# Optimization experiments

Measured on AMD Instinct MI355X. Metric: run time of the kernel, lower is better.

The kernel has to match this reference:

```python
import jax, jax.numpy as jnp
import numpy as np

NUM_EMBEDDINGS = 512
EMBEDDING_DIM = 64
COMMITMENT_COST = 0.25


def setup_inputs() -> dict:
    key = jax.random.key(0)
    k1, k2 = jax.random.split(key)
    inputs = jax.random.normal(k1, (32, EMBEDDING_DIM, 64, 64), dtype=jnp.float32)
    # nn.Embedding weight init: uniform(-1/K, 1/K)
    weight = jax.random.uniform(
        k2, (NUM_EMBEDDINGS, EMBEDDING_DIM), dtype=jnp.float32,
        minval=-1.0 / NUM_EMBEDDINGS, maxval=1.0 / NUM_EMBEDDINGS)
    return {"inputs": inputs, "weight": weight}


def reference(inputs, weight):
    # NCHW -> NHWC
    x = jnp.transpose(inputs, (0, 2, 3, 1))
    B, H, W, D = x.shape
    flat = x.reshape(-1, D)  # [N, D]
    # squared L2 distances to each code: [N, K]
    distances = (jnp.sum(flat * flat, axis=1, keepdims=True)
                 - 2.0 * flat @ weight.T
                 + jnp.sum(weight * weight, axis=1))
    idx = jnp.argmin(distances, axis=1)  # [N]
    # one-hot @ weight == gather (one-hot entries are exactly 0/1)
    quantized = jnp.take(weight, idx, axis=0).reshape(B, H, W, D)
    e_latent_loss = jnp.mean((jax.lax.stop_gradient(quantized) - x) ** 2)
    q_latent_loss = jnp.mean((quantized - jax.lax.stop_gradient(x)) ** 2)
    loss = q_latent_loss + COMMITMENT_COST * e_latent_loss
    # straight-through estimator
    quantized_st = x + jax.lax.stop_gradient(quantized - x)
    discrete_latent = idx.reshape(B, H, W)
    quantized_out = jnp.transpose(quantized_st, (0, 3, 1, 2))  # NHWC -> NCHW
    return discrete_latent, quantized_out, loss
```

## Files before the change

### kernel.cpp

```cpp
#include <hip/hip_runtime.h>

typedef unsigned long long ull;

#define NUM_K   512
#define DIM     64
#define N_ROWS  (32 * 64 * 64)
#define HW      4096
#define CHW     (64 * 4096)

#define IDX_OFF  0
#define Q_OFF    N_ROWS
#define LOSS_OFF (N_ROWS + 32 * 64 * 4096)

#define TILE_R  256
#define RS      68
#define CAP     8

#define WK1S    1.0e-4f
#define WK2S    2.0e-5f

#define WS_FRAG_LO   16384
#define WS_W2_OFF    32768
#define WS_SW_OFF    33280
#define WS_LSL_BYTE  135168
#define WS_NEED      139264

typedef __attribute__((ext_vector_type(8))) short bf16x8;
typedef __attribute__((ext_vector_type(4))) float f32x4;

#define NP_SUMSQ64(SRC, DST)                                                   \
    do {                                                                       \
        float r_[8];                                                           \
        _Pragma("unroll")                                                      \
        for (int j_ = 0; j_ < 8; ++j_) r_[j_] = __fmul_rn((SRC)[j_], (SRC)[j_]); \
        _Pragma("unroll")                                                      \
        for (int i_ = 8; i_ < 64; i_ += 8) {                                   \
            _Pragma("unroll")                                                  \
            for (int j_ = 0; j_ < 8; ++j_)                                     \
                r_[j_] = __fadd_rn(r_[j_], __fmul_rn((SRC)[i_ + j_], (SRC)[i_ + j_])); \
        }                                                                      \
        (DST) = __fadd_rn(__fadd_rn(__fadd_rn(r_[0], r_[1]), __fadd_rn(r_[2], r_[3])), \
                          __fadd_rn(__fadd_rn(r_[4], r_[5]), __fadd_rn(r_[6], r_[7]))); \
    } while (0)

__device__ __forceinline__ unsigned bf16rn(float f) {
    unsigned u = __float_as_uint(f);
    return (u + 0x7fffu + ((u >> 16) & 1u)) >> 16;
}
__device__ __forceinline__ float bf2f(unsigned h) { return __uint_as_float(h << 16); }
__device__ __forceinline__ unsigned pk2(float lo, float hi) {
    return bf16rn(lo) | (bf16rn(hi) << 16);
}

__device__ __forceinline__ float evald(const float* __restrict__ xr,
                                       const float* __restrict__ wc,
                                       float A, float w2c) {
    float m = 0.0f;
    #pragma unroll
    for (int d = 0; d < DIM; ++d) m = __fmaf_rn(xr[d], wc[d], m);
    return __fadd_rn(__fsub_rn(A, __fmul_rn(2.0f, m)), w2c);
}

__global__ void vq_prep(const float* __restrict__ weight, unsigned* __restrict__ ws) {
    const int c = blockIdx.x * 64 + threadIdx.x;
    const float* wr = weight + c * DIM;
    float wv[DIM];
    #pragma unroll
    for (int d = 0; d < DIM; d += 4) {
        float4 t4 = *(const float4*)&wr[d];
        wv[d] = t4.x; wv[d + 1] = t4.y; wv[d + 2] = t4.z; wv[d + 3] = t4.w;
    }
    float s; NP_SUMSQ64(wv, s);
    ((float*)(ws + WS_W2_OFF))[c] = s;
    float sa = 0.0f;
    #pragma unroll
    for (int d = 0; d < DIM; ++d) sa = __fadd_rn(sa, fabsf(wv[d]));
    ((float*)(ws + WS_SW_OFF))[c] = sa * 1.0002f + 1e-7f;

    const int tb = (c >> 4) * 512;
    const int ls = (c & 15) * 4;
    #pragma unroll
    for (int g = 0; g < 8; ++g) {
        int base = tb + (g >> 2) * 256 + (g & 3) * 64 + ls;
        unsigned hu[4], lu[4];
        #pragma unroll
        for (int p = 0; p < 4; ++p) {
            float e0 = wv[8 * g + 2 * p], e1 = wv[8 * g + 2 * p + 1];
            unsigned h0 = bf16rn(e0), h1 = bf16rn(e1);
            float r0 = __fsub_rn(e0, bf2f(h0));
            float r1 = __fsub_rn(e1, bf2f(h1));
            hu[p] = h0 | (h1 << 16);
            lu[p] = bf16rn(r0) | (bf16rn(r1) << 16);
        }
        *(uint4*)&ws[base] = make_uint4(hu[0], hu[1], hu[2], hu[3]);
        *(uint4*)&ws[WS_FRAG_LO + base] = make_uint4(lu[0], lu[1], lu[2], lu[3]);
    }
}

__global__ __launch_bounds__(512, 4) void vq_mfma2(const float* __restrict__ x_in,
                                                   const float* __restrict__ weight,
                                                   const unsigned* __restrict__ frg,
                                                   const float* __restrict__ w2g,
                                                   const float* __restrict__ swg,
                                                   double* __restrict__ lslots,
                                                   float* __restrict__ out) {
    __shared__ float xlds[TILE_R * RS];
    __shared__ float Arow[TILE_R];
    __shared__ float maxx[TILE_R];
    __shared__ int   cntL[TILE_R];
    __shared__ unsigned short listL[TILE_R * CAP];
    __shared__ int   ilds[TILE_R];
    __shared__ float wsum[8];

    const int tid   = threadIdx.x;
    const int lane  = tid & 63;
    const int wid   = tid >> 6;
    const int wbase = wid * 32;
    const int qid   = lane >> 4;
    const int l15   = lane & 15;

    const int rowbase = blockIdx.x * TILE_R;
    const int b       = rowbase >> 12;
    const int hw0     = rowbase & 4095;
    const float* xb   = x_in + (size_t)b * CHW + hw0;

    #pragma unroll
    for (int it = 0; it < 8; ++it) {
        int e = it * 512 + tid;
        int d = e >> 6, r4 = (e & 63) << 2;
        float4 v = *(const float4*)(xb + d * HW + r4);
        xlds[(r4 + 0) * RS + d] = v.x;
        xlds[(r4 + 1) * RS + d] = v.y;
        xlds[(r4 + 2) * RS + d] = v.z;
        xlds[(r4 + 3) * RS + d] = v.w;
    }
    if (tid < TILE_R) cntL[tid] = 0;
    __syncthreads();

    if (tid < TILE_R) {
        const float* src = &xlds[tid * RS];
        float s; NP_SUMSQ64(src, s);
        Arow[tid] = s;
        float mx = 0.0f;
        #pragma unroll
        for (int d = 0; d < DIM; ++d) mx = fmaxf(mx, fabsf(src[d]));
        maxx[tid] = mx;
    }

    bf16x8 afh[2][2], afl[2][2];
    #pragma unroll
    for (int rt = 0; rt < 2; ++rt) {
        int r = wbase + 16 * rt + l15;
        #pragma unroll
        for (int h = 0; h < 2; ++h) {
            int kb = h * 32 + qid * 8;
            float4 xa = *(const float4*)&xlds[r * RS + kb];
            float4 xc = *(const float4*)&xlds[r * RS + kb + 4];
            float xs[8] = {xa.x, xa.y, xa.z, xa.w, xc.x, xc.y, xc.z, xc.w};
            union { unsigned u[4]; bf16x8 v; } ch, cl;
            #pragma unroll
            for (int p = 0; p < 4; ++p) {
                float e0 = xs[2 * p], e1 = xs[2 * p + 1];
                unsigned h0 = bf16rn(e0), h1 = bf16rn(e1);
                float r0 = __fsub_rn(e0, bf2f(h0));
                float r1 = __fsub_rn(e1, bf2f(h1));
                ch.u[p] = h0 | (h1 << 16);
                cl.u[p] = bf16rn(r0) | (bf16rn(r1) << 16);
            }
            afh[rt][h] = ch.v;
            afl[rt][h] = cl.v;
        }
    }
    __syncthreads();

    float wk1r[2][4], tmin[2][4];
    #pragma unroll
    for (int rt = 0; rt < 2; ++rt)
        #pragma unroll
        for (int rg = 0; rg < 4; ++rg) {
            wk1r[rt][rg] = WK1S * maxx[wbase + 16 * rt + 4 * qid + rg];
            tmin[rt][rg] = 3.4e38f;
        }

    const unsigned* fh  = frg + lane * 4;
    const unsigned* flo = frg + WS_FRAG_LO + lane * 4;
    float swrun = 0.0f;

    for (int q = 0; q < 4; ++q) {
        #pragma unroll
        for (int sc = 0; sc < 2; ++sc) {
            f32x4 acc[2][4] = {};
            #pragma unroll
            for (int jx = 0; jx < 4; ++jx) {
                const int tb2 = ((q * 2 + sc) * 4 + jx) * 512;
                bf16x8 bh0 = *(const bf16x8*)&fh[tb2];
                bf16x8 bh1 = *(const bf16x8*)&fh[tb2 + 256];
                bf16x8 bl0 = *(const bf16x8*)&flo[tb2];
                bf16x8 bl1 = *(const bf16x8*)&flo[tb2 + 256];
                #pragma unroll
                for (int rt = 0; rt < 2; ++rt) {
                    acc[rt][jx] = __builtin_amdgcn_mfma_f32_16x16x32_bf16(afh[rt][0], bh0, acc[rt][jx], 0, 0, 0);
                    acc[rt][jx] = __builtin_amdgcn_mfma_f32_16x16x32_bf16(afh[rt][1], bh1, acc[rt][jx], 0, 0, 0);
                    acc[rt][jx] = __builtin_amdgcn_mfma_f32_16x16x32_bf16(afl[rt][0], bh0, acc[rt][jx], 0, 0, 0);
                    acc[rt][jx] = __builtin_amdgcn_mfma_f32_16x16x32_bf16(afl[rt][1], bh1, acc[rt][jx], 0, 0, 0);
                    acc[rt][jx] = __builtin_amdgcn_mfma_f32_16x16x32_bf16(afh[rt][0], bl0, acc[rt][jx], 0, 0, 0);
                    acc[rt][jx] = __builtin_amdgcn_mfma_f32_16x16x32_bf16(afh[rt][1], bl1, acc[rt][jx], 0, 0, 0);
                }
            }

            float tl[2][4], swv[4], swm = 0.0f;
            #pragma unroll
            for (int rt = 0; rt < 2; ++rt)
                #pragma unroll
                for (int rg = 0; rg < 4; ++rg) tl[rt][rg] = 3.4e38f;
            #pragma unroll
            for (int jx = 0; jx < 4; ++jx) {
                int c = q * 128 + (sc * 4 + jx) * 16 + l15;
                float w2hv = 0.5f * w2g[c];
                float sv = swg[c];
                swv[jx] = sv; swm = fmaxf(swm, sv);
                #pragma unroll
                for (int rt = 0; rt < 2; ++rt)
                    #pragma unroll
                    for (int rg = 0; rg < 4; ++rg) {
                        float t = __fsub_rn(w2hv, acc[rt][jx][rg]);
                        acc[rt][jx][rg] = t;
                        tl[rt][rg] = fminf(tl[rt][rg], t);
                    }
            }
            #pragma unroll
            for (int mk = 1; mk <= 8; mk <<= 1) {
                #pragma unroll
                for (int rt = 0; rt < 2; ++rt)
                    #pragma unroll
                    for (int rg = 0; rg < 4; ++rg)
                        tl[rt][rg] = fminf(tl[rt][rg], __shfl_xor(tl[rt][rg], mk));
                swm = fmaxf(swm, __shfl_xor(swm, mk));
            }
            swrun = fmaxf(swrun, swm);
            #pragma unroll
            for (int rt = 0; rt < 2; ++rt)
                #pragma unroll
                for (int rg = 0; rg < 4; ++rg)
                    tmin[rt][rg] = fminf(tmin[rt][rg], tl[rt][rg]);

            #pragma unroll
            for (int rt = 0; rt < 2; ++rt)
                #pragma unroll
                for (int rg = 0; rg < 4; ++rg) {
                    float gate = __fmaf_rn(wk1r[rt][rg], swm + swrun, tmin[rt][rg] + WK2S);
                    if (tl[rt][rg] <= gate) {
                        #pragma unroll
                        for (int jx = 0; jx < 4; ++jx) {
                            float thr = __fmaf_rn(wk1r[rt][rg], swv[jx] + swrun, tmin[rt][rg] + WK2S);
                            if (acc[rt][jx][rg] <= thr) {
                                int r = wbase + 16 * rt + 4 * qid + rg;
                                int c = q * 128 + (sc * 4 + jx) * 16 + l15;
                                int cn = atomicAdd(&cntL[r], 1);
                                if (cn < CAP) listL[r * CAP + cn] = (unsigned short)c;
                            }
                        }
                    }
                }
        }
    }

    __syncthreads();

    if (lane < 32) {
        const int r   = wbase + lane;
        const int cnt = cntL[r];
        if (cnt >= 1 && cnt <= CAP) {
            int bi;
            if (cnt == 1) {
                bi = listL[r * CAP];
            } else {
                const float* xr = &xlds[r * RS];
                const float  A  = Arow[r];
                float bd = 3.4e38f; bi = 1 << 30;
                for (int t2 = 0; t2 < cnt; ++t2) {
                    int c = listL[r * CAP + t2];
                    float d2 = evald(xr, weight + c * DIM, A, w2g[c]);
                    if (d2 < bd || (d2 == bd && c < bi)) { bd = d2; bi = c; }
                }
            }
            ilds[r] = bi;
            out[IDX_OFF + rowbase + r] = (float)bi;
        }
    }
    for (int rr = 0; rr < 32; ++rr) {
        int r   = wbase + rr;
        int cnt = cntL[r];
        if (cnt < 1 || cnt > CAP) {
            const float* xr = &xlds[r * RS];
            const float  A  = Arow[r];
            float bd = 3.4e38f; int bi = 1 << 30;
            #pragma unroll
            for (int t2 = 0; t2 < 8; ++t2) {
                int c = t2 * 64 + lane;
                float d2 = evald(xr, weight + c * DIM, A, w2g[c]);
                if (d2 < bd || (d2 == bd && c < bi)) { bd = d2; bi = c; }
            }
            ull key = ((ull)__float_as_uint(bd) << 32) | (unsigned)bi;
            #pragma unroll
            for (int mk = 1; mk <= 32; mk <<= 1) {
                ull o = __shfl_xor(key, mk);
                if (o < key) key = o;
            }
            if (lane == 0) {
                int bi2 = (int)(key & 0xffffffffu);
                ilds[r] = bi2;
                out[IDX_OFF + rowbase + r] = (float)bi2;
            }
        }
    }
    __syncthreads();

    const int row = wbase + (lane & 31);
    const int dh  = (lane >> 5) << 5;
    const float* xr2 = &xlds[row * RS + dh];
    const float* wr2 = weight + ilds[row] * DIM + dh;
    float* ob = out + Q_OFF + (size_t)b * CHW + hw0 + row;
    float lsum = 0.0f;
    #pragma unroll
    for (int t2 = 0; t2 < 8; ++t2) {
        float4 xv  = *(const float4*)&xr2[4 * t2];
        float4 wv2 = *(const float4*)&wr2[4 * t2];
        float dd;
        dd = __fsub_rn(wv2.x, xv.x); ob[(size_t)(dh + 4 * t2 + 0) * HW] = __fadd_rn(xv.x, dd); lsum = fmaf(dd, dd, lsum);
        dd = __fsub_rn(wv2.y, xv.y); ob[(size_t)(dh + 4 * t2 + 1) * HW] = __fadd_rn(xv.y, dd); lsum = fmaf(dd, dd, lsum);
        dd = __fsub_rn(wv2.z, xv.z); ob[(size_t)(dh + 4 * t2 + 2) * HW] = __fadd_rn(xv.z, dd); lsum = fmaf(dd, dd, lsum);
        dd = __fsub_rn(wv2.w, xv.w); ob[(size_t)(dh + 4 * t2 + 3) * HW] = __fadd_rn(xv.w, dd); lsum = fmaf(dd, dd, lsum);
    }
    #pragma unroll
    for (int off = 32; off > 0; off >>= 1) lsum += __shfl_down(lsum, off);
    if (lane == 0) wsum[wid] = lsum;
    __syncthreads();
    if (tid == 0) {
        double s = 0.0;
        #pragma unroll
        for (int i = 0; i < 8; ++i) s += (double)wsum[i];
        lslots[blockIdx.x] = s;
    }
}

__global__ void vq_finalize4(const double* __restrict__ lslots,
                             float* __restrict__ out) {
    double s = 0.0;
    for (int i = threadIdx.x; i < 512; i += 64) s += lslots[i];
    #pragma unroll
    for (int off = 32; off > 0; off >>= 1) s += __shfl_down(s, off);
    if (threadIdx.x == 0) {
        double m = s / 8388608.0;
        out[LOSS_OFF] = (float)(m + 0.25 * m);
    }
}

#define R1RS      68
#define R1CAP     16
#define WK1       0.018f
#define WK2       2.5e-4f

__global__ __launch_bounds__(512, 2) void vq_mfma(const float* __restrict__ x_in,
                                                  const float* __restrict__ weight,
                                                  double* __restrict__ lslots,
                                                  float* __restrict__ out) {
    __shared__ float xlds[TILE_R * R1RS];
    __shared__ unsigned bfr[NUM_K * 32];
    __shared__ float w2all[NUM_K];
    __shared__ float w2h[NUM_K];
    __shared__ float sumw[NUM_K];
    __shared__ float Arow[TILE_R];
    __shared__ float maxx[TILE_R];
    __shared__ int   cntL[TILE_R];
    __shared__ unsigned short listL[TILE_R * R1CAP];
    __shared__ int   ilds[TILE_R];
    __shared__ float wsum[8];

    const int tid   = threadIdx.x;
    const int lane  = tid & 63;
    const int wid   = tid >> 6;
    const int wbase = wid * 32;
    const int qid   = lane >> 4;
    const int l15   = lane & 15;

    const int rowbase = blockIdx.x * TILE_R;
    const int b       = rowbase >> 12;
    const int hw0     = rowbase & 4095;
    const float* xb   = x_in + (size_t)b * CHW + hw0;

    #pragma unroll
    for (int it = 0; it < 8; ++it) {
        int id  = it * 512 + tid;
        int row = id & 255, g = id >> 8;
        const float* gp = xb + g * 4 * HW + row;
        float4 v = make_float4(gp[0], gp[HW], gp[2 * HW], gp[3 * HW]);
        *(float4*)&xlds[row * R1RS + g * 4] = v;
    }
    {
        const int c = tid;
        const float* wr = weight + c * DIM;
        float wv[DIM];
        #pragma unroll
        for (int d = 0; d < DIM; d += 4) {
            float4 t4 = *(const float4*)&wr[d];
            wv[d] = t4.x; wv[d + 1] = t4.y; wv[d + 2] = t4.z; wv[d + 3] = t4.w;
        }
        float s; NP_SUMSQ64(wv, s);
        w2all[c] = s;
        w2h[c]   = 0.5f * s;
        float sa = 0.0f;
        #pragma unroll
        for (int d = 0; d < DIM; ++d) sa = __fadd_rn(sa, fabsf(wv[d]));
        sumw[c] = sa * 1.0002f + 1e-7f;
        const int tb = (c >> 4) * 512;
        const int ls = (c & 15) * 4;
        #pragma unroll
        for (int g = 0; g < 8; ++g) {
            int base = tb + (g >> 2) * 256 + (g & 3) * 64 + ls;
            uint4 pw = make_uint4(pk2(wv[8 * g + 0], wv[8 * g + 1]),
                                  pk2(wv[8 * g + 2], wv[8 * g + 3]),
                                  pk2(wv[8 * g + 4], wv[8 * g + 5]),
                                  pk2(wv[8 * g + 6], wv[8 * g + 7]));
            *(uint4*)&bfr[base] = pw;
        }
    }
    if (tid < TILE_R) cntL[tid] = 0;
    __syncthreads();

    if (tid < TILE_R) {
        const float* src = &xlds[tid * R1RS];
        float s; NP_SUMSQ64(src, s);
        Arow[tid] = s;
        float mx = 0.0f;
        #pragma unroll
        for (int d = 0; d < DIM; ++d) mx = fmaxf(mx, fabsf(src[d]));
        maxx[tid] = mx;
    }

    bf16x8 afr[2][2];
    #pragma unroll
    for (int rt = 0; rt < 2; ++rt) {
        int r = wbase + 16 * rt + l15;
        #pragma unroll
        for (int h = 0; h < 2; ++h) {
            int kb = h * 32 + qid * 8;
            float4 xa  = *(const float4*)&xlds[r * R1RS + kb];
            float4 xc  = *(const float4*)&xlds[r * R1RS + kb + 4];
            union { unsigned u[4]; bf16x8 v; } cv;
            cv.u[0] = pk2(xa.x, xa.y); cv.u[1] = pk2(xa.z, xa.w);
            cv.u[2] = pk2(xc.x, xc.y); cv.u[3] = pk2(xc.z, xc.w);
            afr[rt][h] = cv.v;
        }
    }
    __syncthreads();

    float wk1r[2][4], tmin[2][4];
    #pragma unroll
    for (int rt = 0; rt < 2; ++rt)
        #pragma unroll
        for (int rg = 0; rg < 4; ++rg) {
            wk1r[rt][rg] = WK1 * maxx[wbase + 16 * rt + 4 * qid + rg];
            tmin[rt][rg] = 3.4e38f;
        }

    const int lane4 = lane * 4;
    for (int q = 0; q < 4; ++q) {
        f32x4 acc[2][8] = {};
        #pragma unroll
        for (int j = 0; j < 8; ++j) {
            int tb2 = (q * 8 + j) * 512;
            bf16x8 bb0 = *(const bf16x8*)&bfr[tb2 + lane4];
            bf16x8 bb1 = *(const bf16x8*)&bfr[tb2 + 256 + lane4];
            acc[0][j] = __builtin_amdgcn_mfma_f32_16x16x32_bf16(afr[0][0], bb0, acc[0][j], 0, 0, 0);
            acc[0][j] = __builtin_amdgcn_mfma_f32_16x16x32_bf16(afr[0][1], bb1, acc[0][j], 0, 0, 0);
            acc[1][j] = __builtin_amdgcn_mfma_f32_16x16x32_bf16(afr[1][0], bb0, acc[1][j], 0, 0, 0);
            acc[1][j] = __builtin_amdgcn_mfma_f32_16x16x32_bf16(afr[1][1], bb1, acc[1][j], 0, 0, 0);
        }

        const int k0 = q * 128;
        float swv[8], tl[2][4];
        #pragma unroll
        for (int rt = 0; rt < 2; ++rt)
            #pragma unroll
            for (int rg = 0; rg < 4; ++rg) tl[rt][rg] = 3.4e38f;
        #pragma unroll
        for (int j = 0; j < 8; ++j) {
            int c = k0 + j * 16 + l15;
            float w2hv = w2h[c];
            swv[j] = sumw[c];
            #pragma unroll
            for (int rt = 0; rt < 2; ++rt)
                #pragma unroll
                for (int rg = 0; rg < 4; ++rg) {
                    float t = w2hv - acc[rt][j][rg];
                    acc[rt][j][rg] = t;
                    tl[rt][rg] = fminf(tl[rt][rg], t);
                }
        }
        #pragma unroll
        for (int mk = 1; mk <= 8; mk <<= 1)
            #pragma unroll
            for (int rt = 0; rt < 2; ++rt)
                #pragma unroll
                for (int rg = 0; rg < 4; ++rg)
                    tl[rt][rg] = fminf(tl[rt][rg], __shfl_xor(tl[rt][rg], mk));
        float thr0[2][4];
        #pragma unroll
        for (int rt = 0; rt < 2; ++rt)
            #pragma unroll
            for (int rg = 0; rg < 4; ++rg) {
                tmin[rt][rg] = fminf(tmin[rt][rg], tl[rt][rg]);
                thr0[rt][rg] = tmin[rt][rg] + WK2;
            }
        float swmax = swv[0];
        #pragma unroll
        for (int j = 1; j < 8; ++j) swmax = fmaxf(swmax, swv[j]);

        #pragma unroll
        for (int rt = 0; rt < 2; ++rt)
            #pragma unroll
            for (int rg = 0; rg < 4; ++rg) {
                if (tl[rt][rg] <= __fmaf_rn(wk1r[rt][rg], swmax, thr0[rt][rg])) {
                    #pragma unroll
                    for (int j = 0; j < 8; ++j) {
                        if (acc[rt][j][rg] <= __fmaf_rn(wk1r[rt][rg], swv[j], thr0[rt][rg])) {
                            int r  = wbase + 16 * rt + 4 * qid + rg;
                            int c  = k0 + j * 16 + l15;
                            int cn = atomicAdd(&cntL[r], 1);
                            if (cn < R1CAP) listL[r * R1CAP + cn] = (unsigned short)c;
                        }
                    }
                }
            }
    }

    __syncthreads();

    if (lane < 32) {
        const int r   = wbase + lane;
        const int cnt = cntL[r];
        if (cnt >= 1 && cnt <= R1CAP) {
            const float* xr = &xlds[r * R1RS];
            const float  A  = Arow[r];
            float bd = 3.4e38f; int bi = 1 << 30;
            for (int t2 = 0; t2 < cnt; ++t2) {
                int c = listL[r * R1CAP + t2];
                float d2 = evald(xr, weight + c * DIM, A, w2all[c]);
                if (d2 < bd || (d2 == bd && c < bi)) { bd = d2; bi = c; }
            }
            ilds[r] = bi;
            out[IDX_OFF + rowbase + r] = (float)bi;
        }
    }
    for (int rr = 0; rr < 32; ++rr) {
        int r   = wbase + rr;
        int cnt = cntL[r];
        if (cnt < 1 || cnt > R1CAP) {
            const float* xr = &xlds[r * R1RS];
            const float  A  = Arow[r];
            float bd = 3.4e38f; int bi = 1 << 30;
            #pragma unroll
            for (int t2 = 0; t2 < 8; ++t2) {
                int c = t2 * 64 + lane;
                float d2 = evald(xr, weight + c * DIM, A, w2all[c]);
                if (d2 < bd || (d2 == bd && c < bi)) { bd = d2; bi = c; }
            }
            ull key = ((ull)__float_as_uint(bd) << 32) | (unsigned)bi;
            #pragma unroll
            for (int mk = 1; mk <= 32; mk <<= 1) {
                ull o = __shfl_xor(key, mk);
                if (o < key) key = o;
            }
            if (lane == 0) {
                int bi2 = (int)(key & 0xffffffffu);
                ilds[r] = bi2;
                out[IDX_OFF + rowbase + r] = (float)bi2;
            }
        }
    }
    __syncthreads();

    const int row = wbase + (lane & 31);
    const int dh  = (lane >> 5) << 5;
    const float* xr2 = &xlds[row * R1RS + dh];
    const float* wr2 = weight + ilds[row] * DIM + dh;
    float* ob = out + Q_OFF + (size_t)b * CHW + hw0 + row;
    float lsum = 0.0f;
    #pragma unroll
    for (int t2 = 0; t2 < 8; ++t2) {
        float4 xv  = *(const float4*)&xr2[4 * t2];
        float4 wv2 = *(const float4*)&wr2[4 * t2];
        float dd;
        dd = __fsub_rn(wv2.x, xv.x); ob[(size_t)(dh + 4 * t2 + 0) * HW] = __fadd_rn(xv.x, dd); lsum = fmaf(dd, dd, lsum);
        dd = __fsub_rn(wv2.y, xv.y); ob[(size_t)(dh + 4 * t2 + 1) * HW] = __fadd_rn(xv.y, dd); lsum = fmaf(dd, dd, lsum);
        dd = __fsub_rn(wv2.z, xv.z); ob[(size_t)(dh + 4 * t2 + 2) * HW] = __fadd_rn(xv.z, dd); lsum = fmaf(dd, dd, lsum);
        dd = __fsub_rn(wv2.w, xv.w); ob[(size_t)(dh + 4 * t2 + 3) * HW] = __fadd_rn(xv.w, dd); lsum = fmaf(dd, dd, lsum);
    }
    #pragma unroll
    for (int off = 32; off > 0; off >>= 1) lsum += __shfl_down(lsum, off);
    if (lane == 0) wsum[wid] = lsum;
    __syncthreads();
    if (tid == 0) {
        double s = 0.0;
        #pragma unroll
        for (int i = 0; i < 8; ++i) s += (double)wsum[i];
        lslots[blockIdx.x] = s;
    }
}

__global__ void vq_zero(double* __restrict__ loss_acc) {
    if (threadIdx.x == 0) *loss_acc = 0.0;
}

__global__ __launch_bounds__(256) void vq_fused(const float* __restrict__ x_in,
                                                const float* __restrict__ weight,
                                                double* __restrict__ loss_acc,
                                                float* __restrict__ out) {
    __shared__ float w2s[NUM_K];
    for (int k = threadIdx.x; k < NUM_K; k += 256) {
        const float* wk = weight + k * DIM;
        float s; NP_SUMSQ64(wk, s);
        w2s[k] = s;
    }
    __syncthreads();

    const int n  = blockIdx.x * 256 + threadIdx.x;
    const int b  = n >> 12;
    const int hw = n & 4095;
    const float* xp = x_in + b * CHW + hw;
    float x[DIM];
    #pragma unroll
    for (int d = 0; d < DIM; ++d) x[d] = xp[d * HW];

    float A; NP_SUMSQ64(x, A);

    float best = 3.4e38f;
    int   bi   = 0;
    for (int k = 0; k < NUM_K; k += 4) {
        const float* w0 = weight + k * DIM;
        float m0 = 0.f, m1 = 0.f, m2 = 0.f, m3 = 0.f;
        #pragma unroll
        for (int d = 0; d < DIM; ++d) {
            float xd = x[d];
            m0 = __fmaf_rn(xd, w0[d],           m0);
            m1 = __fmaf_rn(xd, w0[DIM + d],     m1);
            m2 = __fmaf_rn(xd, w0[2 * DIM + d], m2);
            m3 = __fmaf_rn(xd, w0[3 * DIM + d], m3);
        }
        float d0 = __fadd_rn(__fsub_rn(A, __fmul_rn(2.0f, m0)), w2s[k]);
        float d1 = __fadd_rn(__fsub_rn(A, __fmul_rn(2.0f, m1)), w2s[k + 1]);
        float d2 = __fadd_rn(__fsub_rn(A, __fmul_rn(2.0f, m2)), w2s[k + 2]);
        float d3 = __fadd_rn(__fsub_rn(A, __fmul_rn(2.0f, m3)), w2s[k + 3]);
        if (d0 < best) { best = d0; bi = k; }
        if (d1 < best) { best = d1; bi = k + 1; }
        if (d2 < best) { best = d2; bi = k + 2; }
        if (d3 < best) { best = d3; bi = k + 3; }
    }
    const int idx = bi;

    out[IDX_OFF + n] = (float)idx;
    const float* qrow = weight + idx * DIM;
    float* oq = out + Q_OFF + b * CHW + hw;
    float lsum = 0.0f;
    #pragma unroll
    for (int d = 0; d < DIM; ++d) {
        float xd   = xp[d * HW];
        float diff = __fsub_rn(qrow[d], xd);
        oq[d * HW] = __fadd_rn(xd, diff);
        lsum = fmaf(diff, diff, lsum);
    }
    #pragma unroll
    for (int off = 32; off > 0; off >>= 1) lsum += __shfl_down(lsum, off);
    __shared__ float wsum[4];
    if ((threadIdx.x & 63) == 0) wsum[threadIdx.x >> 6] = lsum;
    __syncthreads();
    if (threadIdx.x == 0)
        atomicAdd(loss_acc, (double)((wsum[0] + wsum[1]) + (wsum[2] + wsum[3])));
}

__global__ void vq_finalize(const double* __restrict__ loss_acc,
                            float* __restrict__ out) {
    double m = *loss_acc / 8388608.0;
    out[LOSS_OFF] = (float)(m + 0.25 * m);
}

extern "C" void kernel_launch(void* const* d_in, const int* in_sizes, int n_in,
                              void* d_out, int out_size, void* d_ws, size_t ws_size,
                              hipStream_t stream) {
    const float* x = (const float*)d_in[0];
    const float* w = (const float*)d_in[1];
    float* out = (float*)d_out;

    if (ws_size >= WS_NEED) {
        unsigned* ws32 = (unsigned*)d_ws;
        const float* w2g = (const float*)(ws32 + WS_W2_OFF);
        const float* swg = (const float*)(ws32 + WS_SW_OFF);
        double* lslots = (double*)((char*)d_ws + WS_LSL_BYTE);
        vq_prep<<<8, 64, 0, stream>>>(w, ws32);
        vq_mfma2<<<N_ROWS / TILE_R, 512, 0, stream>>>(x, w, ws32, w2g, swg, lslots, out);
        vq_finalize4<<<1, 64, 0, stream>>>(lslots, out);
    } else if (ws_size >= 512 * sizeof(double)) {
        double* lslots = (double*)d_ws;
        vq_mfma<<<N_ROWS / TILE_R, 512, 0, stream>>>(x, w, lslots, out);
        vq_finalize4<<<1, 64, 0, stream>>>(lslots, out);
    } else {
        double* loss_acc = (double*)d_ws;
        vq_zero<<<1, 64, 0, stream>>>(loss_acc);
        vq_fused<<<512, 256, 0, stream>>>(x, w, loss_acc, out);
        vq_finalize<<<1, 1, 0, stream>>>(loss_acc, out);
    }
}
```

Measured before the change: 169.3 us.

## Halve row tile, precompute global code-norm max, fuse loss finalize via atomics

Replaces the 256-row, 512-thread main kernel with a 128-row, 256-thread variant launched on twice as many blocks. It also precomputes the maximum code abs-sum once in the prep kernel, so the per-chunk shuffle reductions and running-max gate arithmetic become a single fixed threshold per row. The prep kernel becomes one 512-thread block that zeroes a loss accumulator and counter. The separate finalize launch is removed: each block atomically adds its loss, and the last block writes the final value. Trade-offs are a looser, fixed candidate threshold that may admit more refinement candidates, and double atomics on a single global address.

```diff
diff --git a/kernel.cpp b/kernel.cpp
--- a/kernel.cpp
+++ b/kernel.cpp
@@ -12,9 +12,10 @@
 #define Q_OFF    N_ROWS
 #define LOSS_OFF (N_ROWS + 32 * 64 * 4096)
 
-#define TILE_R  256
 #define RS      68
 #define CAP     8
+#define TILE_R3 128
+#define NBLK3   (N_ROWS / TILE_R3)
 
 #define WK1S    1.0e-4f
 #define WK2S    2.0e-5f
@@ -22,7 +23,9 @@
 #define WS_FRAG_LO   16384
 #define WS_W2_OFF    32768
 #define WS_SW_OFF    33280
-#define WS_LSL_BYTE  135168
+#define WS_SWMAX_OFF 33792
+#define WS_LOSS_BYTE 135168
+#define WS_CNT_BYTE  135176
 #define WS_NEED      139264
 
 typedef __attribute__((ext_vector_type(8))) short bf16x8;
@@ -61,8 +64,10 @@
     return __fadd_rn(__fsub_rn(A, __fmul_rn(2.0f, m)), w2c);
 }
 
-__global__ void vq_prep(const float* __restrict__ weight, unsigned* __restrict__ ws) {
-    const int c = blockIdx.x * 64 + threadIdx.x;
+__global__ __launch_bounds__(512) void vq_prep(const float* __restrict__ weight,
+                                               unsigned* __restrict__ ws) {
+    __shared__ float red[512];
+    const int c = threadIdx.x;
     const float* wr = weight + c * DIM;
     float wv[DIM];
     #pragma unroll
@@ -75,7 +80,9 @@
     float sa = 0.0f;
     #pragma unroll
     for (int d = 0; d < DIM; ++d) sa = __fadd_rn(sa, fabsf(wv[d]));
-    ((float*)(ws + WS_SW_OFF))[c] = sa * 1.0002f + 1e-7f;
+    float sv = sa * 1.0002f + 1e-7f;
+    ((float*)(ws + WS_SW_OFF))[c] = sv;
+    red[c] = sv;
 
     const int tb = (c >> 4) * 512;
     const int ls = (c & 15) * 4;
@@ -95,22 +102,32 @@
         *(uint4*)&ws[base] = make_uint4(hu[0], hu[1], hu[2], hu[3]);
         *(uint4*)&ws[WS_FRAG_LO + base] = make_uint4(lu[0], lu[1], lu[2], lu[3]);
     }
-}
-
-__global__ __launch_bounds__(512, 4) void vq_mfma2(const float* __restrict__ x_in,
+    __syncthreads();
+    #pragma unroll
+    for (int st = 256; st > 0; st >>= 1) {
+        if (c < st) red[c] = fmaxf(red[c], red[c + st]);
+        __syncthreads();
+    }
+    if (c == 0) {
+        ((float*)(ws + WS_SWMAX_OFF))[0] = red[0];
+        *(double*)((char*)ws + WS_LOSS_BYTE) = 0.0;
+        *(unsigned*)((char*)ws + WS_CNT_BYTE) = 0u;
+    }
+}
+
+__global__ __launch_bounds__(256, 4) void vq_mfma3(const float* __restrict__ x_in,
                                                    const float* __restrict__ weight,
                                                    const unsigned* __restrict__ frg,
                                                    const float* __restrict__ w2g,
-                                                   const float* __restrict__ swg,
-                                                   double* __restrict__ lslots,
+                                                   unsigned* __restrict__ wsraw,
                                                    float* __restrict__ out) {
-    __shared__ float xlds[TILE_R * RS];
-    __shared__ float Arow[TILE_R];
-    __shared__ float maxx[TILE_R];
-    __shared__ int   cntL[TILE_R];
-    __shared__ unsigned short listL[TILE_R * CAP];
-    __shared__ int   ilds[TILE_R];
-    __shared__ float wsum[8];
+    __shared__ float xlds[TILE_R3 * RS];
+    __shared__ float Arow[TILE_R3];
+    __shared__ float maxx[TILE_R3];
+    __shared__ int   cntL[TILE_R3];
+    __shared__ unsigned short listL[TILE_R3 * CAP];
+    __shared__ int   ilds[TILE_R3];
+    __shared__ float wsum[4];
 
     const int tid   = threadIdx.x;
     const int lane  = tid & 63;
@@ -119,25 +136,23 @@
     const int qid   = lane >> 4;
     const int l15   = lane & 15;
 
-    const int rowbase = blockIdx.x * TILE_R;
+    const int rowbase = blockIdx.x * TILE_R3;
     const int b       = rowbase >> 12;
     const int hw0     = rowbase & 4095;
     const float* xb   = x_in + (size_t)b * CHW + hw0;
 
     #pragma unroll
     for (int it = 0; it < 8; ++it) {
-        int e = it * 512 + tid;
-        int d = e >> 6, r4 = (e & 63) << 2;
-        float4 v = *(const float4*)(xb + d * HW + r4);
-        xlds[(r4 + 0) * RS + d] = v.x;
-        xlds[(r4 + 1) * RS + d] = v.y;
-        xlds[(r4 + 2) * RS + d] = v.z;
-        xlds[(r4 + 3) * RS + d] = v.w;
-    }
-    if (tid < TILE_R) cntL[tid] = 0;
-    __syncthreads();
-
-    if (tid < TILE_R) {
+        int id  = it * 256 + tid;
+        int row = id & 127, g = id >> 7;
+        const float* gp = xb + g * 4 * HW + row;
+        float4 v = make_float4(gp[0], gp[HW], gp[2 * HW], gp[3 * HW]);
+        *(float4*)&xlds[row * RS + g * 4] = v;
+    }
+    if (tid < TILE_R3) cntL[tid] = 0;
+    __syncthreads();
+
+    if (tid < TILE_R3) {
         const float* src = &xlds[tid * RS];
         float s; NP_SUMSQ64(src, s);
         Arow[tid] = s;
@@ -173,18 +188,19 @@
     }
     __syncthreads();
 
-    float wk1r[2][4], tmin[2][4];
+    const float SWMAX = ((const float*)(frg + WS_SWMAX_OFF))[0];
+    float gthr[2][4], thr[2][4];
     #pragma unroll
     for (int rt = 0; rt < 2; ++rt)
         #pragma unroll
         for (int rg = 0; rg < 4; ++rg) {
-            wk1r[rt][rg] = WK1S * maxx[wbase + 16 * rt + 4 * qid + rg];
-            tmin[rt][rg] = 3.4e38f;
+            float wk1 = WK1S * maxx[wbase + 16 * rt + 4 * qid + rg];
+            gthr[rt][rg] = __fmaf_rn(wk1, 2.0f * SWMAX, WK2S);
+            thr[rt][rg]  = 3.4e38f;
         }
 
     const unsigned* fh  = frg + lane * 4;
     const unsigned* flo = frg + WS_FRAG_LO + lane * 4;
-    float swrun = 0.0f;
 
     for (int q = 0; q < 4; ++q) {
         #pragma unroll
@@ -208,7 +224,7 @@
                 }
             }
 
-            float tl[2][4], swv[4], swm = 0.0f;
+            float tl[2][4];
             #pragma unroll
             for (int rt = 0; rt < 2; ++rt)
                 #pragma unroll
@@ -217,8 +233,6 @@
             for (int jx = 0; jx < 4; ++jx) {
                 int c = q * 128 + (sc * 4 + jx) * 16 + l15;
                 float w2hv = 0.5f * w2g[c];
-                float sv = swg[c];
-                swv[jx] = sv; swm = fmaxf(swm, sv);
                 #pragma unroll
                 for (int rt = 0; rt < 2; ++rt)
                     #pragma unroll
@@ -229,31 +243,27 @@
                     }
             }
             #pragma unroll
-            for (int mk = 1; mk <= 8; mk <<= 1) {
+            for (int mk = 1; mk <= 8; mk <<= 1)
                 #pragma unroll
                 for (int rt = 0; rt < 2; ++rt)
                     #pragma unroll
                     for (int rg = 0; rg < 4; ++rg)
                         tl[rt][rg] = fminf(tl[rt][rg], __shfl_xor(tl[rt][rg], mk));
-                swm = fmaxf(swm, __shfl_xor(swm, mk));
-            }
-            swrun = fmaxf(swrun, swm);
             #pragma unroll
             for (int rt = 0; rt < 2; ++rt)
                 #pragma unroll
                 for (int rg = 0; rg < 4; ++rg)
-                    tmin[rt][rg] = fminf(tmin[rt][rg], tl[rt][rg]);
+                    thr[rt][rg] = fminf(thr[rt][rg],
+                                        __fadd_rn(tl[rt][rg], gthr[rt][rg]));
 
             #pragma unroll
             for (int rt = 0; rt < 2; ++rt)
                 #pragma unroll
                 for (int rg = 0; rg < 4; ++rg) {
-                    float gate = __fmaf_rn(wk1r[rt][rg], swm + swrun, tmin[rt][rg] + WK2S);
-                    if (tl[rt][rg] <= gate) {
+                    if (tl[rt][rg] <= thr[rt][rg]) {
                         #pragma unroll
                         for (int jx = 0; jx < 4; ++jx) {
-                            float thr = __fmaf_rn(wk1r[rt][rg], swv[jx] + swrun, tmin[rt][rg] + WK2S);
-                            if (acc[rt][jx][rg] <= thr) {
+                            if (acc[rt][jx][rg] <= thr[rt][rg]) {
                                 int r = wbase + 16 * rt + 4 * qid + rg;
                                 int c = q * 128 + (sc * 4 + jx) * 16 + l15;
                                 int cn = atomicAdd(&cntL[r], 1);
@@ -339,24 +349,21 @@
     if (tid == 0) {
         double s = 0.0;
         #pragma unroll
-        for (int i = 0; i < 8; ++i) s += (double)wsum[i];
-        lslots[blockIdx.x] = s;
-    }
-}
-
-__global__ void vq_finalize4(const double* __restrict__ lslots,
-                             float* __restrict__ out) {
-    double s = 0.0;
-    for (int i = threadIdx.x; i < 512; i += 64) s += lslots[i];
-    #pragma unroll
-    for (int off = 32; off > 0; off >>= 1) s += __shfl_down(s, off);
-    if (threadIdx.x == 0) {
-        double m = s / 8388608.0;
-        out[LOSS_OFF] = (float)(m + 0.25 * m);
-    }
-}
-
-#define R1RS      68
+        for (int i = 0; i < 4; ++i) s += (double)wsum[i];
+        double* lossacc = (double*)((char*)wsraw + WS_LOSS_BYTE);
+        unsigned* cnt   = (unsigned*)((char*)wsraw + WS_CNT_BYTE);
+        atomicAdd(lossacc, s);
+        __threadfence();
+        unsigned old = atomicAdd(cnt, 1u);
+        if (old == NBLK3 - 1) {
+            double tot = atomicAdd(lossacc, 0.0);
+            double m = tot / 8388608.0;
+            out[LOSS_OFF] = (float)(m + 0.25 * m);
+        }
+    }
+}
+
+#define TILE_R    256
 #define R1CAP     16
 #define WK1       0.018f
 #define WK2       2.5e-4f
@@ -365,7 +372,7 @@
                                                   const float* __restrict__ weight,
                                                   double* __restrict__ lslots,
                                                   float* __restrict__ out) {
-    __shared__ float xlds[TILE_R * R1RS];
+    __shared__ float xlds[TILE_R * RS];
     __shared__ unsigned bfr[NUM_K * 32];
     __shared__ float w2all[NUM_K];
     __shared__ float w2h[NUM_K];
@@ -395,7 +402,7 @@
         int row = id & 255, g = id >> 8;
         const float* gp = xb + g * 4 * HW + row;
         float4 v = make_float4(gp[0], gp[HW], gp[2 * HW], gp[3 * HW]);
-        *(float4*)&xlds[row * R1RS + g * 4] = v;
+        *(float4*)&xlds[row * RS + g * 4] = v;
     }
     {
         const int c = tid;
@@ -429,7 +436,7 @@
     __syncthreads();
 
     if (tid < TILE_R) {
-        const float* src = &xlds[tid * R1RS];
+        const float* src = &xlds[tid * RS];
         float s; NP_SUMSQ64(src, s);
         Arow[tid] = s;
         float mx = 0.0f;
@@ -445,8 +452,8 @@
         #pragma unroll
         for (int h = 0; h < 2; ++h) {
             int kb = h * 32 + qid * 8;
-            float4 xa  = *(const float4*)&xlds[r * R1RS + kb];
-            float4 xc  = *(const float4*)&xlds[r * R1RS + kb + 4];
+            float4 xa  = *(const float4*)&xlds[r * RS + kb];
+            float4 xc  = *(const float4*)&xlds[r * RS + kb + 4];
             union { unsigned u[4]; bf16x8 v; } cv;
             cv.u[0] = pk2(xa.x, xa.y); cv.u[1] = pk2(xa.z, xa.w);
             cv.u[2] = pk2(xc.x, xc.y); cv.u[3] = pk2(xc.z, xc.w);
@@ -541,7 +548,7 @@
         const int r   = wbase + lane;
         const int cnt = cntL[r];
         if (cnt >= 1 && cnt <= R1CAP) {
-            const float* xr = &xlds[r * R1RS];
+            const float* xr = &xlds[r * RS];
             const float  A  = Arow[r];
             float bd = 3.4e38f; int bi = 1 << 30;
             for (int t2 = 0; t2 < cnt; ++t2) {
@@ -557,7 +564,7 @@
         int r   = wbase + rr;
         int cnt = cntL[r];
         if (cnt < 1 || cnt > R1CAP) {
-            const float* xr = &xlds[r * R1RS];
+            const float* xr = &xlds[r * RS];
             const float  A  = Arow[r];
             float bd = 3.4e38f; int bi = 1 << 30;
             #pragma unroll
@@ -583,7 +590,7 @@
 
     const int row = wbase + (lane & 31);
     const int dh  = (lane >> 5) << 5;
-    const float* xr2 = &xlds[row * R1RS + dh];
+    const float* xr2 = &xlds[row * RS + dh];
     const float* wr2 = weight + ilds[row] * DIM + dh;
     float* ob = out + Q_OFF + (size_t)b * CHW + hw0 + row;
     float lsum = 0.0f;
@@ -606,6 +613,18 @@
         #pragma unroll
         for (int i = 0; i < 8; ++i) s += (double)wsum[i];
         lslots[blockIdx.x] = s;
+    }
+}
+
+__global__ void vq_finalize4(const double* __restrict__ lslots,
+                             float* __restrict__ out) {
+    double s = 0.0;
+    for (int i = threadIdx.x; i < 512; i += 64) s += lslots[i];
+    #pragma unroll
+    for (int off = 32; off > 0; off >>= 1) s += __shfl_down(s, off);
+    if (threadIdx.x == 0) {
+        double m = s / 8388608.0;
+        out[LOSS_OFF] = (float)(m + 0.25 * m);
     }
 }
 
@@ -695,11 +714,8 @@
     if (ws_size >= WS_NEED) {
         unsigned* ws32 = (unsigned*)d_ws;
         const float* w2g = (const float*)(ws32 + WS_W2_OFF);
-        const float* swg = (const float*)(ws32 + WS_SW_OFF);
-        double* lslots = (double*)((char*)d_ws + WS_LSL_BYTE);
-        vq_prep<<<8, 64, 0, stream>>>(w, ws32);
-        vq_mfma2<<<N_ROWS / TILE_R, 512, 0, stream>>>(x, w, ws32, w2g, swg, lslots, out);
-        vq_finalize4<<<1, 64, 0, stream>>>(lslots, out);
+        vq_prep<<<1, 512, 0, stream>>>(w, ws32);
+        vq_mfma3<<<NBLK3, 256, 0, stream>>>(x, w, ws32, w2g, ws32, out);
     } else if (ws_size >= 512 * sizeof(double)) {
         double* lslots = (double*)d_ws;
         vq_mfma<<<N_ROWS / TILE_R, 512, 0, stream>>>(x, w, lslots, out);
```

Result: slower. 184.6 us (+9.1%).
